# Performance work log

Hardware: AMD Instinct MI355X
Metric: run time of the kernel (lower is better)

## Reference

```python
import jax, jax.numpy as jnp
import numpy as np

H, F, E_SHARED, E_ROUTED, K = 1024, 4096, 1, 8, 2


def setup_inputs() -> dict:
    key = jax.random.key(0)
    ks = jax.random.split(key, 6)
    x = jax.random.normal(ks[0], (4, 2048, H), dtype=jnp.float32)
    s = 0.02
    shared_up = jax.random.normal(ks[1], (E_SHARED, H, F), dtype=jnp.float32) * s
    shared_down = jax.random.normal(ks[2], (E_SHARED, F, H), dtype=jnp.float32) * s
    routed_up = jax.random.normal(ks[3], (E_ROUTED, H, F), dtype=jnp.float32) * s
    routed_down = jax.random.normal(ks[4], (E_ROUTED, F, H), dtype=jnp.float32) * s
    router_w = jax.random.normal(ks[5], (H, E_ROUTED), dtype=jnp.float32) * s
    return {"x": x, "shared_up": shared_up, "shared_down": shared_down,
            "routed_up": routed_up, "routed_down": routed_down, "router_w": router_w}


def _expert(x, w_up, w_down):
    # ExpertBlock: down(gelu(up(x))), exact (erf) gelu as in torch F.gelu default
    h = jax.nn.gelu(jnp.einsum('bsh,hf->bsf', x, w_up), approximate=False)
    return jnp.einsum('bsf,fh->bsh', h, w_down)


def reference(x, shared_up, shared_down, routed_up, routed_down, router_w):
    # shared experts (always active)
    shared_out = jnp.zeros_like(x)
    for i in range(E_SHARED):
        shared_out = shared_out + _expert(x, shared_up[i], shared_down[i])

    # router: softmax over routed experts, then top-k gating
    probs = jax.nn.softmax(jnp.einsum('bsh,he->bse', x, router_w), axis=-1)
    top_k_prob, top_k_idx = jax.lax.top_k(probs, K)  # [B,S,K]
    # per-expert gate = sum of top-k probs assigned to that expert
    onehot = jax.nn.one_hot(top_k_idx, E_ROUTED, dtype=x.dtype)  # [B,S,K,E]
    gates = jnp.einsum('bsk,bske->bse', top_k_prob, onehot)      # [B,S,E]

    routed_out = jnp.zeros_like(x)
    for e in range(E_ROUTED):  # fixed small loop over experts
        y = _expert(x, routed_up[e], routed_down[e])
        routed_out = routed_out + gates[..., e:e + 1] * y

    return shared_out + routed_out + x
```

## Files before the change

### kernel.cpp

```cpp
#include <hip/hip_runtime.h>
#include <cstdint>
#include <cstddef>

#define HD 1024
#define FF 4096
#define TOK 8192
#define NSEG 9
#define ROWS_ROUTED (TOK*2)
#define ROWS_TOT (ROWS_ROUTED + TOK)

typedef __bf16 bf16;
typedef __bf16 bf16x8 __attribute__((ext_vector_type(8)));
typedef __bf16 bf16x4 __attribute__((ext_vector_type(4)));
typedef float  f32x4  __attribute__((ext_vector_type(4)));

__device__ __forceinline__ void stage16(const void* g, void* l) {
  __builtin_amdgcn_global_load_lds((const __attribute__((address_space(1))) void*)g,
                                   (__attribute__((address_space(3))) void*)l,
                                   16, 0, 0);
}

__device__ __forceinline__ unsigned short bf_bits(float v) {
  bf16 b = (bf16)v;
  return __builtin_bit_cast(unsigned short, b);
}

__global__ void k_init_meta(int* meta) {
  int t = threadIdx.x;
  if (t < 64) meta[t] = 0;
}

__global__ void k_convert_x(const float* __restrict__ x, bf16* __restrict__ xbf) {
  int i = blockIdx.x*256 + threadIdx.x;
  float4 v = reinterpret_cast<const float4*>(x)[i];
  ushort4 u;
  u.x = bf_bits(v.x); u.y = bf_bits(v.y); u.z = bf_bits(v.z); u.w = bf_bits(v.w);
  reinterpret_cast<ushort4*>(xbf)[i] = u;
}

__global__ void k_tcvt(const float* __restrict__ routed, const float* __restrict__ shared_,
                       bf16* __restrict__ dst, int R, int C) {
  int e = blockIdx.z;
  const float* src = (e < 8) ? (routed + (size_t)e*R*C) : shared_;
  bf16* d = dst + (size_t)e*R*C;
  __shared__ float lds[64][65];
  int r0 = blockIdx.y*64, c0 = blockIdx.x*64;
  int t = threadIdx.x;
  int tr = t>>4, tc4 = (t&15)*4;
  #pragma unroll
  for (int i=0;i<4;i++) {
    float4 v = *reinterpret_cast<const float4*>(src + (size_t)(r0+tr+i*16)*C + c0 + tc4);
    lds[tr+i*16][tc4+0]=v.x; lds[tr+i*16][tc4+1]=v.y;
    lds[tr+i*16][tc4+2]=v.z; lds[tr+i*16][tc4+3]=v.w;
  }
  __syncthreads();
  #pragma unroll
  for (int i=0;i<4;i++) {
    int oc = tr + i*16;
    ushort4 u;
    u.x = bf_bits(lds[tc4+0][oc]);
    u.y = bf_bits(lds[tc4+1][oc]);
    u.z = bf_bits(lds[tc4+2][oc]);
    u.w = bf_bits(lds[tc4+3][oc]);
    *reinterpret_cast<ushort4*>(d + (size_t)(c0+oc)*R + r0 + tc4) = u;
  }
}

__global__ void k_router(const float* __restrict__ x, const float* __restrict__ rw,
                         int* __restrict__ rtE, float* __restrict__ rtG,
                         int* __restrict__ meta) {
  __shared__ float rwl[HD*8];
  int t = threadIdx.x;
  for (int i=t;i<HD*8/4;i+=256)
    reinterpret_cast<float4*>(rwl)[i] = reinterpret_cast<const float4*>(rw)[i];
  __syncthreads();
  int wv = t>>6, lane = t&63;
  int tk = blockIdx.x*4 + wv;
  const float* xr = x + (size_t)tk*HD;
  float a[8] = {0,0,0,0,0,0,0,0};
  for (int i=0;i<HD/64;i++) {
    int h = lane + i*64;
    float xv = xr[h];
    const float* r = rwl + h*8;
    #pragma unroll
    for (int e=0;e<8;e++) a[e] = fmaf(xv, r[e], a[e]);
  }
  #pragma unroll
  for (int e=0;e<8;e++) {
    for (int s=32;s>0;s>>=1) a[e] += __shfl_xor(a[e], s, 64);
  }
  if (lane==0) {
    float mx = a[0];
    #pragma unroll
    for (int e=1;e<8;e++) mx = fmaxf(mx, a[e]);
    float p[8]; float den = 0.f;
    #pragma unroll
    for (int e=0;e<8;e++) { p[e] = expf(a[e]-mx); den += p[e]; }
    int i0 = 0;
    #pragma unroll
    for (int e=1;e<8;e++) if (p[e] > p[i0]) i0 = e;
    int i1 = (i0==0)?1:0;
    #pragma unroll
    for (int e=0;e<8;e++) if (e!=i0 && p[e] > p[i1]) i1 = e;
    float inv = 1.f/den;
    rtE[tk*2] = i0; rtE[tk*2+1] = i1;
    rtG[tk*2] = p[i0]*inv; rtG[tk*2+1] = p[i1]*inv;
    atomicAdd(&meta[i0], 1);
    atomicAdd(&meta[i1], 1);
  }
}

__global__ void k_prefix(int* meta) {
  if (threadIdx.x == 0) {
    int off = 0;
    for (int e=0;e<8;e++) { meta[16+e] = off; meta[32+e] = meta[e]; off += meta[e]; }
    meta[16+8] = ROWS_ROUTED;
    meta[32+8] = TOK;
  }
}

__global__ void k_scatter(const int* __restrict__ rtE, const float* __restrict__ rtG,
                          int* __restrict__ meta, int* __restrict__ tok,
                          float* __restrict__ gate, int* __restrict__ trow) {
  int t = blockIdx.x*256 + threadIdx.x;
  int e0 = rtE[t*2], e1 = rtE[t*2+1];
  float g0 = rtG[t*2], g1 = rtG[t*2+1];
  int p0 = atomicAdd(&meta[8+e0], 1);
  int r0 = meta[16+e0] + p0;
  tok[r0] = t; gate[r0] = g0; trow[t*2] = r0;
  int p1 = atomicAdd(&meta[8+e1], 1);
  int r1 = meta[16+e1] + p1;
  tok[r1] = t; gate[r1] = g1; trow[t*2+1] = r1;
  tok[ROWS_ROUTED + t] = t; gate[ROWS_ROUTED + t] = 1.0f;
}

__global__ void k_combine(const float* __restrict__ x, const bf16* __restrict__ dbuf,
                          const int* __restrict__ trow, float* __restrict__ out) {
  int tkn = blockIdx.x;
  int t = threadIdx.x;
  int r0 = trow[tkn*2], r1 = trow[tkn*2+1];
  int h = t*4;
  float4 xv = *reinterpret_cast<const float4*>(x + (size_t)tkn*HD + h);
  bf16x4 a = *reinterpret_cast<const bf16x4*>(dbuf + (size_t)(ROWS_ROUTED+tkn)*HD + h);
  bf16x4 b = *reinterpret_cast<const bf16x4*>(dbuf + (size_t)r0*HD + h);
  bf16x4 c = *reinterpret_cast<const bf16x4*>(dbuf + (size_t)r1*HD + h);
  float4 o;
  o.x = xv.x + (float)a[0] + (float)b[0] + (float)c[0];
  o.y = xv.y + (float)a[1] + (float)b[1] + (float)c[1];
  o.z = xv.z + (float)a[2] + (float)b[2] + (float)c[2];
  o.w = xv.w + (float)a[3] + (float)b[3] + (float)c[3];
  *reinterpret_cast<float4*>(out + (size_t)tkn*HD + h) = o;
}


__global__ __launch_bounds__(256,2) void k_gemm_up(
    const bf16* __restrict__ xbf, const bf16* __restrict__ wupT,
    bf16* __restrict__ hbuf, const int* __restrict__ tok,
    const int* __restrict__ meta, int ch, int FC, int ntiles)
{
  int bx = blockIdx.x;
  int bps = 64*ntiles;
  int seg = bx / bps; int rem = bx % bps;
  int mt = rem / ntiles, nt = rem % ntiles;
  int rows = (seg<8)? meta[32+seg] : TOK;
  if (mt*128 >= rows) return;
  int segoff = meta[16+seg];
  int rowbase = mt*128;

  __shared__ __align__(16) bf16 Alds[2][128*32];
  __shared__ __align__(16) bf16 Blds[2][128*32];

  const int t = threadIdx.x;
  const int lane = t & 63, w = t >> 6;

  int lr0 = t>>2, lr1 = 64 + (t>>2);
  int gr0 = rowbase + lr0; if (gr0 >= rows) gr0 = rowbase;
  int gr1 = rowbase + lr1; if (gr1 >= rows) gr1 = rowbase;
  int tok0 = tok[segoff + gr0], tok1 = tok[segoff + gr1];
  int kswz = ((t&3) ^ ((t>>3)&3)) * 8;
  const bf16* gA0 = xbf + (size_t)tok0*HD + kswz;
  const bf16* gA1 = xbf + (size_t)tok1*HD + kswz;
  const bf16* wb = wupT + (size_t)seg*FF*HD;
  int f0 = ch*FC + nt*128;
  const bf16* gB0 = wb + (size_t)(f0 + lr0)*HD + kswz;
  const bf16* gB1 = wb + (size_t)(f0 + lr1)*HD + kswz;

  char* AldsB = (char*)Alds; char* BldsB = (char*)Blds;
  const int stoff = w*1024;

  const int slotb = ((lane>>4) ^ (((lane&15)>>1)&3)) * 16;
  const int Afo = ((w>>1)*64 + (lane&15))*64 + slotb;
  const int Bfo = ((w&1)*64 + (lane&15))*64 + slotb;

  f32x4 acc[4][4] = {};

  stage16(gA0, AldsB + stoff);
  stage16(gA1, AldsB + 4096 + stoff);
  stage16(gB0, BldsB + stoff);
  stage16(gB1, BldsB + 4096 + stoff);
  __syncthreads();

  int cur = 0;
  for (int k0=32; k0<HD; k0+=32) {
    char* an = AldsB + (cur^1)*8192;
    char* bn = BldsB + (cur^1)*8192;
    stage16(gA0 + k0, an + stoff);
    stage16(gA1 + k0, an + 4096 + stoff);
    stage16(gB0 + k0, bn + stoff);
    stage16(gB1 + k0, bn + 4096 + stoff);
    const char* Ab = AldsB + cur*8192 + Afo;
    const char* Bb = BldsB + cur*8192 + Bfo;
    bf16x8 af[4], bfr[4];
    #pragma unroll
    for (int m=0;m<4;m++) af[m]  = *reinterpret_cast<const bf16x8*>(Ab + m*1024);
    #pragma unroll
    for (int n=0;n<4;n++) bfr[n] = *reinterpret_cast<const bf16x8*>(Bb + n*1024);
    #pragma unroll
    for (int m=0;m<4;m++)
      #pragma unroll
      for (int n=0;n<4;n++)
        acc[m][n] = __builtin_amdgcn_mfma_f32_16x16x32_bf16(bfr[n], af[m], acc[m][n], 0,0,0);
    __syncthreads();
    cur ^= 1;
  }
  {
    const char* Ab = AldsB + cur*8192 + Afo;
    const char* Bb = BldsB + cur*8192 + Bfo;
    bf16x8 af[4], bfr[4];
    #pragma unroll
    for (int m=0;m<4;m++) af[m]  = *reinterpret_cast<const bf16x8*>(Ab + m*1024);
    #pragma unroll
    for (int n=0;n<4;n++) bfr[n] = *reinterpret_cast<const bf16x8*>(Bb + n*1024);
    #pragma unroll
    for (int m=0;m<4;m++)
      #pragma unroll
      for (int n=0;n<4;n++)
        acc[m][n] = __builtin_amdgcn_mfma_f32_16x16x32_bf16(bfr[n], af[m], acc[m][n], 0,0,0);
  }

  const int lrm = lane&15, lq = lane>>4;
  #pragma unroll
  for (int m=0;m<4;m++) {
    int rl = (w>>1)*64 + m*16 + lrm;
    int gr = rowbase + rl;
    if (gr >= rows) continue;
    bf16* hrow = hbuf + (size_t)(segoff+gr)*FC + nt*128 + (w&1)*64 + lq*4;
    #pragma unroll
    for (int n=0;n<4;n++) {
      bf16x4 u;
      #pragma unroll
      for (int j=0;j<4;j++) {
        float v = acc[m][n][j];
        v = 0.5f*v*(1.0f + erff(v*0.70710678118654752f));
        u[j] = (bf16)v;
      }
      *reinterpret_cast<bf16x4*>(hrow + n*16) = u;
    }
  }
}

__global__ __launch_bounds__(256,2) void k_gemm_down(
    const bf16* __restrict__ hbuf, const bf16* __restrict__ wdnT,
    bf16* __restrict__ dbuf, const float* __restrict__ gate,
    const int* __restrict__ meta, int ch, int FC, int first)
{
  int bx = blockIdx.x;
  int seg = bx >> 9;
  int rem = bx & 511;
  int mt = rem >> 3, nt = rem & 7;
  int rows = (seg<8)? meta[32+seg] : TOK;
  if (mt*128 >= rows) return;
  int segoff = meta[16+seg];
  int rowbase = mt*128;

  __shared__ __align__(16) bf16 Alds[2][128*32];
  __shared__ __align__(16) bf16 Blds[2][128*32];
  __shared__ float gateL[128];

  const int t = threadIdx.x;
  const int lane = t & 63, w = t >> 6;

  if (t < 128) {
    int gr = rowbase + t; if (gr >= rows) gr = rows - 1;
    gateL[t] = gate[segoff + gr];
  }

  int lr0 = t>>2, lr1 = 64 + (t>>2);
  int kswz = ((t&3) ^ ((t>>3)&3)) * 8;
  const bf16* gA0 = hbuf + (size_t)(segoff + rowbase + lr0)*FC + kswz;
  const bf16* gA1 = hbuf + (size_t)(segoff + rowbase + lr1)*FC + kswz;
  const bf16* wb = wdnT + (size_t)seg*HD*FF;
  int h0 = nt*128;
  const bf16* gB0 = wb + (size_t)(h0 + lr0)*FF + ch*FC + kswz;
  const bf16* gB1 = wb + (size_t)(h0 + lr1)*FF + ch*FC + kswz;

  char* AldsB = (char*)Alds; char* BldsB = (char*)Blds;
  const int stoff = w*1024;

  const int slotb = ((lane>>4) ^ (((lane&15)>>1)&3)) * 16;
  const int Afo = ((w>>1)*64 + (lane&15))*64 + slotb;
  const int Bfo = ((w&1)*64 + (lane&15))*64 + slotb;

  f32x4 acc[4][4] = {};

  stage16(gA0, AldsB + stoff);
  stage16(gA1, AldsB + 4096 + stoff);
  stage16(gB0, BldsB + stoff);
  stage16(gB1, BldsB + 4096 + stoff);
  __syncthreads();

  int cur = 0;
  for (int k0=32; k0<FC; k0+=32) {
    char* an = AldsB + (cur^1)*8192;
    char* bn = BldsB + (cur^1)*8192;
    stage16(gA0 + k0, an + stoff);
    stage16(gA1 + k0, an + 4096 + stoff);
    stage16(gB0 + k0, bn + stoff);
    stage16(gB1 + k0, bn + 4096 + stoff);
    const char* Ab = AldsB + cur*8192 + Afo;
    const char* Bb = BldsB + cur*8192 + Bfo;
    bf16x8 af[4], bfr[4];
    #pragma unroll
    for (int m=0;m<4;m++) af[m]  = *reinterpret_cast<const bf16x8*>(Ab + m*1024);
    #pragma unroll
    for (int n=0;n<4;n++) bfr[n] = *reinterpret_cast<const bf16x8*>(Bb + n*1024);
    #pragma unroll
    for (int m=0;m<4;m++)
      #pragma unroll
      for (int n=0;n<4;n++)
        acc[m][n] = __builtin_amdgcn_mfma_f32_16x16x32_bf16(bfr[n], af[m], acc[m][n], 0,0,0);
    __syncthreads();
    cur ^= 1;
  }
  {
    const char* Ab = AldsB + cur*8192 + Afo;
    const char* Bb = BldsB + cur*8192 + Bfo;
    bf16x8 af[4], bfr[4];
    #pragma unroll
    for (int m=0;m<4;m++) af[m]  = *reinterpret_cast<const bf16x8*>(Ab + m*1024);
    #pragma unroll
    for (int n=0;n<4;n++) bfr[n] = *reinterpret_cast<const bf16x8*>(Bb + n*1024);
    #pragma unroll
    for (int m=0;m<4;m++)
      #pragma unroll
      for (int n=0;n<4;n++)
        acc[m][n] = __builtin_amdgcn_mfma_f32_16x16x32_bf16(bfr[n], af[m], acc[m][n], 0,0,0);
  }

  const int lrm = lane&15, lq = lane>>4;
  #pragma unroll
  for (int m=0;m<4;m++) {
    int rl = (w>>1)*64 + m*16 + lrm;
    int gr = rowbase + rl;
    if (gr >= rows) continue;
    float g = gateL[rl];
    bf16* drow = dbuf + (size_t)(segoff+gr)*HD + nt*128 + (w&1)*64 + lq*4;
    #pragma unroll
    for (int n=0;n<4;n++) {
      bf16x4 u;
      if (first) {
        #pragma unroll
        for (int j=0;j<4;j++) u[j] = (bf16)(acc[m][n][j]*g);
      } else {
        bf16x4 o = *reinterpret_cast<const bf16x4*>(drow + n*16);
        #pragma unroll
        for (int j=0;j<4;j++) u[j] = (bf16)((float)o[j] + acc[m][n][j]*g);
      }
      *reinterpret_cast<bf16x4*>(drow + n*16) = u;
    }
  }
}

struct Layout {
  size_t xbf, wupT, wdnT, hbuf, dbuf, tok, gate, trow, rtE, rtG, meta, total;
};

static inline Layout make_layout(size_t FC) {
  Layout L; size_t o = 0;
  auto al = [&](size_t b){ o = (o+255)&~(size_t)255; size_t r=o; o+=b; return r; };
  L.xbf  = al((size_t)TOK*HD*2);
  L.wupT = al((size_t)NSEG*FF*HD*2);
  L.wdnT = al((size_t)NSEG*FF*HD*2);
  L.hbuf = al((size_t)ROWS_TOT*FC*2);
  L.dbuf = al((size_t)ROWS_TOT*HD*2);
  L.tok  = al((size_t)ROWS_TOT*4);
  L.gate = al((size_t)ROWS_TOT*4);
  L.trow = al((size_t)TOK*2*4);
  L.rtE  = al((size_t)TOK*2*4);
  L.rtG  = al((size_t)TOK*2*4);
  L.meta = al(256*4);
  L.total = o;
  return L;
}

extern "C" void kernel_launch(void* const* d_in, const int* in_sizes, int n_in,
                              void* d_out, int out_size, void* d_ws, size_t ws_size,
                              hipStream_t stream) {
  const float* x           = (const float*)d_in[0];
  const float* shared_up   = (const float*)d_in[1];
  const float* shared_down = (const float*)d_in[2];
  const float* routed_up   = (const float*)d_in[3];
  const float* routed_down = (const float*)d_in[4];
  const float* router_w    = (const float*)d_in[5];
  float* out = (float*)d_out;

  size_t FC = 4096;
  while (FC > 256 && make_layout(FC).total > ws_size) FC >>= 1;
  Layout L = make_layout(FC);

  char* ws = (char*)d_ws;
  bf16*  xbf  = (bf16*)(ws + L.xbf);
  bf16*  wupT = (bf16*)(ws + L.wupT);
  bf16*  wdnT = (bf16*)(ws + L.wdnT);
  bf16*  hbuf = (bf16*)(ws + L.hbuf);
  bf16*  dbuf = (bf16*)(ws + L.dbuf);
  int*   tok  = (int*)(ws + L.tok);
  float* gate = (float*)(ws + L.gate);
  int*   trow = (int*)(ws + L.trow);
  int*   rtE  = (int*)(ws + L.rtE);
  float* rtG  = (float*)(ws + L.rtG);
  int*   meta = (int*)(ws + L.meta);

  k_init_meta<<<1, 64, 0, stream>>>(meta);
  k_convert_x<<<TOK*HD/1024, 256, 0, stream>>>(x, xbf);
  k_tcvt<<<dim3(FF/64, HD/64, NSEG), 256, 0, stream>>>(routed_up, shared_up, wupT, HD, FF);
  k_tcvt<<<dim3(HD/64, FF/64, NSEG), 256, 0, stream>>>(routed_down, shared_down, wdnT, FF, HD);
  k_router<<<TOK/4, 256, 0, stream>>>(x, router_w, rtE, rtG, meta);
  k_prefix<<<1, 64, 0, stream>>>(meta);
  k_scatter<<<TOK/256, 256, 0, stream>>>(rtE, rtG, meta, tok, gate, trow);

  int ntiles = (int)(FC/128);
  int fc = (int)FC;
  for (int ch = 0; ch*fc < FF; ++ch) {
    k_gemm_up<<<NSEG*64*ntiles, 256, 0, stream>>>(xbf, wupT, hbuf, tok, meta, ch, fc, ntiles);
    k_gemm_down<<<NSEG*64*8, 256, 0, stream>>>(hbuf, wdnT, dbuf, gate, meta, ch, fc, ch==0 ? 1 : 0);
  }
  k_combine<<<TOK, 256, 0, stream>>>(x, dbuf, trow, out);
}
```

Baseline: 1.044 ms.

## Enlarge GEMM tiles to 256 rows with 512 threads and triple-buffered LDS pipeline

Both expert GEMMs move to 512-thread blocks with 256-row tiles (256x256 for up, 256x128 for down), and the double-buffered LDS loop becomes a 3-stage pipeline with explicit vmcnt waits, raw barriers and raised wave priority around the MFMA block. The FC chunking loop is removed, so the full 4096-wide hidden buffer is always allocated and the down GEMM writes its output once instead of read-modify-writing per chunk. Larger tiles raise arithmetic intensity and deeper prefetch hides load latency, at the cost of more registers and LDS per block, fewer blocks, and a larger workspace requirement with no fallback if ws_size is too small.

```diff
diff --git a/kernel.cpp b/kernel.cpp
--- a/kernel.cpp
+++ b/kernel.cpp
@@ -8,6 +8,9 @@
 #define NSEG 9
 #define ROWS_ROUTED (TOK*2)
 #define ROWS_TOT (ROWS_ROUTED + TOK)
+
+#define BUF_UP 32768
+#define BUF_DN 24576
 
 typedef __bf16 bf16;
 typedef __bf16 bf16x8 __attribute__((ext_vector_type(8)));
@@ -153,98 +156,87 @@
 }
 
 
-__global__ __launch_bounds__(256,2) void k_gemm_up(
+__global__ __launch_bounds__(512,2) void k_gemm_up(
     const bf16* __restrict__ xbf, const bf16* __restrict__ wupT,
     bf16* __restrict__ hbuf, const int* __restrict__ tok,
-    const int* __restrict__ meta, int ch, int FC, int ntiles)
+    const int* __restrict__ meta)
 {
   int bx = blockIdx.x;
-  int bps = 64*ntiles;
-  int seg = bx / bps; int rem = bx % bps;
-  int mt = rem / ntiles, nt = rem % ntiles;
+  int seg = bx >> 9;
+  int rem = bx & 511;
+  int mt = rem >> 4, nt = rem & 15;
   int rows = (seg<8)? meta[32+seg] : TOK;
-  if (mt*128 >= rows) return;
+  if (mt*256 >= rows) return;
   int segoff = meta[16+seg];
-  int rowbase = mt*128;
-
-  __shared__ __align__(16) bf16 Alds[2][128*32];
-  __shared__ __align__(16) bf16 Blds[2][128*32];
+  int rowbase = mt*256;
+
+  __shared__ __align__(16) char lds[3*BUF_UP];
 
   const int t = threadIdx.x;
   const int lane = t & 63, w = t >> 6;
-
-  int lr0 = t>>2, lr1 = 64 + (t>>2);
-  int gr0 = rowbase + lr0; if (gr0 >= rows) gr0 = rowbase;
-  int gr1 = rowbase + lr1; if (gr1 >= rows) gr1 = rowbase;
-  int tok0 = tok[segoff + gr0], tok1 = tok[segoff + gr1];
+  const int wm = w >> 2, wn = w & 3;
+
+  int ar = t>>2;
   int kswz = ((t&3) ^ ((t>>3)&3)) * 8;
-  const bf16* gA0 = xbf + (size_t)tok0*HD + kswz;
-  const bf16* gA1 = xbf + (size_t)tok1*HD + kswz;
+  int gr0 = rowbase + ar;        if (gr0 >= rows) gr0 = rows-1;
+  int gr1 = rowbase + 128 + ar;  if (gr1 >= rows) gr1 = rows-1;
+  const bf16* gA0 = xbf + (size_t)tok[segoff+gr0]*HD + kswz;
+  const bf16* gA1 = xbf + (size_t)tok[segoff+gr1]*HD + kswz;
   const bf16* wb = wupT + (size_t)seg*FF*HD;
-  int f0 = ch*FC + nt*128;
-  const bf16* gB0 = wb + (size_t)(f0 + lr0)*HD + kswz;
-  const bf16* gB1 = wb + (size_t)(f0 + lr1)*HD + kswz;
-
-  char* AldsB = (char*)Alds; char* BldsB = (char*)Blds;
-  const int stoff = w*1024;
-
-  const int slotb = ((lane>>4) ^ (((lane&15)>>1)&3)) * 16;
-  const int Afo = ((w>>1)*64 + (lane&15))*64 + slotb;
-  const int Bfo = ((w&1)*64 + (lane&15))*64 + slotb;
-
-  f32x4 acc[4][4] = {};
-
-  stage16(gA0, AldsB + stoff);
-  stage16(gA1, AldsB + 4096 + stoff);
-  stage16(gB0, BldsB + stoff);
-  stage16(gB1, BldsB + 4096 + stoff);
-  __syncthreads();
-
-  int cur = 0;
-  for (int k0=32; k0<HD; k0+=32) {
-    char* an = AldsB + (cur^1)*8192;
-    char* bn = BldsB + (cur^1)*8192;
-    stage16(gA0 + k0, an + stoff);
-    stage16(gA1 + k0, an + 4096 + stoff);
-    stage16(gB0 + k0, bn + stoff);
-    stage16(gB1 + k0, bn + 4096 + stoff);
-    const char* Ab = AldsB + cur*8192 + Afo;
-    const char* Bb = BldsB + cur*8192 + Bfo;
-    bf16x8 af[4], bfr[4];
-    #pragma unroll
-    for (int m=0;m<4;m++) af[m]  = *reinterpret_cast<const bf16x8*>(Ab + m*1024);
-    #pragma unroll
-    for (int n=0;n<4;n++) bfr[n] = *reinterpret_cast<const bf16x8*>(Bb + n*1024);
-    #pragma unroll
-    for (int m=0;m<4;m++)
+  int f0 = nt*256;
+  const bf16* gB0 = wb + (size_t)(f0 + ar)*HD + kswz;
+  const bf16* gB1 = wb + (size_t)(f0 + 128 + ar)*HD + kswz;
+  const int dA0 = t*16, dA1 = 8192 + t*16, dB0 = 16384 + t*16, dB1 = 24576 + t*16;
+
+  const int sx = ((lane>>4) ^ (((lane&15)>>1)&3)) * 16;
+  const int Afo = (wm*128 + (lane&15))*64 + sx;
+  const int Bfo = 16384 + (wn*64 + (lane&15))*64 + sx;
+
+  f32x4 acc[8][4] = {};
+
+  stage16(gA0,    lds + dA0); stage16(gA1,    lds + dA1);
+  stage16(gB0,    lds + dB0); stage16(gB1,    lds + dB1);
+  stage16(gA0+32, lds + BUF_UP + dA0); stage16(gA1+32, lds + BUF_UP + dA1);
+  stage16(gB0+32, lds + BUF_UP + dB0); stage16(gB1+32, lds + BUF_UP + dB1);
+  asm volatile("s_waitcnt vmcnt(4)" ::: "memory");
+  __builtin_amdgcn_s_barrier();
+  __builtin_amdgcn_sched_barrier(0);
+
+  int cur = 0, nxt = 2;
+  for (int kt = 0; kt < HD/32; ++kt) {
+    if (kt + 2 < HD/32) {
+      int ko = (kt+2)*32;
+      char* nb = lds + nxt*BUF_UP;
+      stage16(gA0+ko, nb + dA0); stage16(gA1+ko, nb + dA1);
+      stage16(gB0+ko, nb + dB0); stage16(gB1+ko, nb + dB1);
+    }
+    const char* cb = lds + cur*BUF_UP;
+    bf16x8 af[8], bfr[4];
+    #pragma unroll
+    for (int m=0;m<8;m++) af[m]  = *reinterpret_cast<const bf16x8*>(cb + Afo + m*1024);
+    #pragma unroll
+    for (int n=0;n<4;n++) bfr[n] = *reinterpret_cast<const bf16x8*>(cb + Bfo + n*1024);
+    __builtin_amdgcn_s_setprio(1);
+    #pragma unroll
+    for (int m=0;m<8;m++)
       #pragma unroll
       for (int n=0;n<4;n++)
         acc[m][n] = __builtin_amdgcn_mfma_f32_16x16x32_bf16(bfr[n], af[m], acc[m][n], 0,0,0);
-    __syncthreads();
-    cur ^= 1;
-  }
-  {
-    const char* Ab = AldsB + cur*8192 + Afo;
-    const char* Bb = BldsB + cur*8192 + Bfo;
-    bf16x8 af[4], bfr[4];
-    #pragma unroll
-    for (int m=0;m<4;m++) af[m]  = *reinterpret_cast<const bf16x8*>(Ab + m*1024);
-    #pragma unroll
-    for (int n=0;n<4;n++) bfr[n] = *reinterpret_cast<const bf16x8*>(Bb + n*1024);
-    #pragma unroll
-    for (int m=0;m<4;m++)
-      #pragma unroll
-      for (int n=0;n<4;n++)
-        acc[m][n] = __builtin_amdgcn_mfma_f32_16x16x32_bf16(bfr[n], af[m], acc[m][n], 0,0,0);
+    __builtin_amdgcn_s_setprio(0);
+    if (kt + 2 < HD/32)       asm volatile("s_waitcnt vmcnt(4)" ::: "memory");
+    else if (kt + 1 < HD/32)  asm volatile("s_waitcnt vmcnt(0)" ::: "memory");
+    __builtin_amdgcn_s_barrier();
+    __builtin_amdgcn_sched_barrier(0);
+    cur = (cur==2)?0:cur+1; nxt = (nxt==2)?0:nxt+1;
   }
 
   const int lrm = lane&15, lq = lane>>4;
   #pragma unroll
-  for (int m=0;m<4;m++) {
-    int rl = (w>>1)*64 + m*16 + lrm;
+  for (int m=0;m<8;m++) {
+    int rl = wm*128 + m*16 + lrm;
     int gr = rowbase + rl;
     if (gr >= rows) continue;
-    bf16* hrow = hbuf + (size_t)(segoff+gr)*FC + nt*128 + (w&1)*64 + lq*4;
+    bf16* hrow = hbuf + (size_t)(segoff+gr)*FF + nt*256 + wn*64 + lq*4;
     #pragma unroll
     for (int n=0;n<4;n++) {
       bf16x4 u;
@@ -259,113 +251,94 @@
   }
 }
 
-__global__ __launch_bounds__(256,2) void k_gemm_down(
+__global__ __launch_bounds__(512,2) void k_gemm_down(
     const bf16* __restrict__ hbuf, const bf16* __restrict__ wdnT,
     bf16* __restrict__ dbuf, const float* __restrict__ gate,
-    const int* __restrict__ meta, int ch, int FC, int first)
+    const int* __restrict__ meta)
 {
   int bx = blockIdx.x;
-  int seg = bx >> 9;
-  int rem = bx & 511;
+  int seg = bx >> 8;
+  int rem = bx & 255;
   int mt = rem >> 3, nt = rem & 7;
   int rows = (seg<8)? meta[32+seg] : TOK;
-  if (mt*128 >= rows) return;
+  if (mt*256 >= rows) return;
   int segoff = meta[16+seg];
-  int rowbase = mt*128;
-
-  __shared__ __align__(16) bf16 Alds[2][128*32];
-  __shared__ __align__(16) bf16 Blds[2][128*32];
-  __shared__ float gateL[128];
+  int rowbase = mt*256;
+
+  __shared__ __align__(16) char lds[3*BUF_DN];
+  __shared__ float gateL[256];
 
   const int t = threadIdx.x;
   const int lane = t & 63, w = t >> 6;
-
-  if (t < 128) {
+  const int wm = w >> 2, wn = w & 3;
+
+  if (t < 256) {
     int gr = rowbase + t; if (gr >= rows) gr = rows - 1;
     gateL[t] = gate[segoff + gr];
   }
 
-  int lr0 = t>>2, lr1 = 64 + (t>>2);
+  int ar = t>>2;
   int kswz = ((t&3) ^ ((t>>3)&3)) * 8;
-  const bf16* gA0 = hbuf + (size_t)(segoff + rowbase + lr0)*FC + kswz;
-  const bf16* gA1 = hbuf + (size_t)(segoff + rowbase + lr1)*FC + kswz;
+  const bf16* gA0 = hbuf + (size_t)(segoff + rowbase + ar)*FF + kswz;
+  const bf16* gA1 = hbuf + (size_t)(segoff + rowbase + 128 + ar)*FF + kswz;
   const bf16* wb = wdnT + (size_t)seg*HD*FF;
   int h0 = nt*128;
-  const bf16* gB0 = wb + (size_t)(h0 + lr0)*FF + ch*FC + kswz;
-  const bf16* gB1 = wb + (size_t)(h0 + lr1)*FF + ch*FC + kswz;
-
-  char* AldsB = (char*)Alds; char* BldsB = (char*)Blds;
-  const int stoff = w*1024;
-
-  const int slotb = ((lane>>4) ^ (((lane&15)>>1)&3)) * 16;
-  const int Afo = ((w>>1)*64 + (lane&15))*64 + slotb;
-  const int Bfo = ((w&1)*64 + (lane&15))*64 + slotb;
-
-  f32x4 acc[4][4] = {};
-
-  stage16(gA0, AldsB + stoff);
-  stage16(gA1, AldsB + 4096 + stoff);
-  stage16(gB0, BldsB + stoff);
-  stage16(gB1, BldsB + 4096 + stoff);
-  __syncthreads();
-
-  int cur = 0;
-  for (int k0=32; k0<FC; k0+=32) {
-    char* an = AldsB + (cur^1)*8192;
-    char* bn = BldsB + (cur^1)*8192;
-    stage16(gA0 + k0, an + stoff);
-    stage16(gA1 + k0, an + 4096 + stoff);
-    stage16(gB0 + k0, bn + stoff);
-    stage16(gB1 + k0, bn + 4096 + stoff);
-    const char* Ab = AldsB + cur*8192 + Afo;
-    const char* Bb = BldsB + cur*8192 + Bfo;
-    bf16x8 af[4], bfr[4];
-    #pragma unroll
-    for (int m=0;m<4;m++) af[m]  = *reinterpret_cast<const bf16x8*>(Ab + m*1024);
-    #pragma unroll
-    for (int n=0;n<4;n++) bfr[n] = *reinterpret_cast<const bf16x8*>(Bb + n*1024);
-    #pragma unroll
-    for (int m=0;m<4;m++)
+  const bf16* gB0 = wb + (size_t)(h0 + ar)*FF + kswz;
+  const int dA0 = t*16, dA1 = 8192 + t*16, dB0 = 16384 + t*16;
+
+  const int sx = ((lane>>4) ^ (((lane&15)>>1)&3)) * 16;
+  const int Afo = (wm*128 + (lane&15))*64 + sx;
+  const int Bfo = 16384 + (wn*32 + (lane&15))*64 + sx;
+
+  f32x4 acc[8][2] = {};
+
+  stage16(gA0,    lds + dA0); stage16(gA1,    lds + dA1); stage16(gB0,    lds + dB0);
+  stage16(gA0+32, lds + BUF_DN + dA0); stage16(gA1+32, lds + BUF_DN + dA1);
+  stage16(gB0+32, lds + BUF_DN + dB0);
+  asm volatile("s_waitcnt vmcnt(3)" ::: "memory");
+  __builtin_amdgcn_s_barrier();
+  __builtin_amdgcn_sched_barrier(0);
+
+  int cur = 0, nxt = 2;
+  for (int kt = 0; kt < FF/32; ++kt) {
+    if (kt + 2 < FF/32) {
+      int ko = (kt+2)*32;
+      char* nb = lds + nxt*BUF_DN;
+      stage16(gA0+ko, nb + dA0); stage16(gA1+ko, nb + dA1); stage16(gB0+ko, nb + dB0);
+    }
+    const char* cb = lds + cur*BUF_DN;
+    bf16x8 af[8], bfr[2];
+    #pragma unroll
+    for (int m=0;m<8;m++) af[m]  = *reinterpret_cast<const bf16x8*>(cb + Afo + m*1024);
+    #pragma unroll
+    for (int n=0;n<2;n++) bfr[n] = *reinterpret_cast<const bf16x8*>(cb + Bfo + n*1024);
+    __builtin_amdgcn_s_setprio(1);
+    #pragma unroll
+    for (int m=0;m<8;m++)
       #pragma unroll
-      for (int n=0;n<4;n++)
+      for (int n=0;n<2;n++)
         acc[m][n] = __builtin_amdgcn_mfma_f32_16x16x32_bf16(bfr[n], af[m], acc[m][n], 0,0,0);
-    __syncthreads();
-    cur ^= 1;
-  }
-  {
-    const char* Ab = AldsB + cur*8192 + Afo;
-    const char* Bb = BldsB + cur*8192 + Bfo;
-    bf16x8 af[4], bfr[4];
-    #pragma unroll
-    for (int m=0;m<4;m++) af[m]  = *reinterpret_cast<const bf16x8*>(Ab + m*1024);
-    #pragma unroll
-    for (int n=0;n<4;n++) bfr[n] = *reinterpret_cast<const bf16x8*>(Bb + n*1024);
-    #pragma unroll
-    for (int m=0;m<4;m++)
-      #pragma unroll
-      for (int n=0;n<4;n++)
-        acc[m][n] = __builtin_amdgcn_mfma_f32_16x16x32_bf16(bfr[n], af[m], acc[m][n], 0,0,0);
+    __builtin_amdgcn_s_setprio(0);
+    if (kt + 2 < FF/32)       asm volatile("s_waitcnt vmcnt(3)" ::: "memory");
+    else if (kt + 1 < FF/32)  asm volatile("s_waitcnt vmcnt(0)" ::: "memory");
+    __builtin_amdgcn_s_barrier();
+    __builtin_amdgcn_sched_barrier(0);
+    cur = (cur==2)?0:cur+1; nxt = (nxt==2)?0:nxt+1;
   }
 
   const int lrm = lane&15, lq = lane>>4;
   #pragma unroll
-  for (int m=0;m<4;m++) {
-    int rl = (w>>1)*64 + m*16 + lrm;
+  for (int m=0;m<8;m++) {
+    int rl = wm*128 + m*16 + lrm;
     int gr = rowbase + rl;
     if (gr >= rows) continue;
     float g = gateL[rl];
-    bf16* drow = dbuf + (size_t)(segoff+gr)*HD + nt*128 + (w&1)*64 + lq*4;
-    #pragma unroll
-    for (int n=0;n<4;n++) {
+    bf16* drow = dbuf + (size_t)(segoff+gr)*HD + nt*128 + wn*32 + lq*4;
+    #pragma unroll
+    for (int n=0;n<2;n++) {
       bf16x4 u;
-      if (first) {
-        #pragma unroll
-        for (int j=0;j<4;j++) u[j] = (bf16)(acc[m][n][j]*g);
-      } else {
-        bf16x4 o = *reinterpret_cast<const bf16x4*>(drow + n*16);
-        #pragma unroll
-        for (int j=0;j<4;j++) u[j] = (bf16)((float)o[j] + acc[m][n][j]*g);
-      }
+      #pragma unroll
+      for (int j=0;j<4;j++) u[j] = (bf16)(acc[m][n][j]*g);
       *reinterpret_cast<bf16x4*>(drow + n*16) = u;
     }
   }
@@ -375,13 +348,13 @@
   size_t xbf, wupT, wdnT, hbuf, dbuf, tok, gate, trow, rtE, rtG, meta, total;
 };
 
-static inline Layout make_layout(size_t FC) {
+static inline Layout make_layout() {
   Layout L; size_t o = 0;
   auto al = [&](size_t b){ o = (o+255)&~(size_t)255; size_t r=o; o+=b; return r; };
   L.xbf  = al((size_t)TOK*HD*2);
   L.wupT = al((size_t)NSEG*FF*HD*2);
   L.wdnT = al((size_t)NSEG*FF*HD*2);
-  L.hbuf = al((size_t)ROWS_TOT*FC*2);
+  L.hbuf = al((size_t)ROWS_TOT*FF*2);
   L.dbuf = al((size_t)ROWS_TOT*HD*2);
   L.tok  = al((size_t)ROWS_TOT*4);
   L.gate = al((size_t)ROWS_TOT*4);
@@ -404,10 +377,7 @@
   const float* router_w    = (const float*)d_in[5];
   float* out = (float*)d_out;
 
-  size_t FC = 4096;
-  while (FC > 256 && make_layout(FC).total > ws_size) FC >>= 1;
-  Layout L = make_layout(FC);
-
+  Layout L = make_layout();
   char* ws = (char*)d_ws;
   bf16*  xbf  = (bf16*)(ws + L.xbf);
   bf16*  wupT = (bf16*)(ws + L.wupT);
@@ -429,11 +399,7 @@
   k_prefix<<<1, 64, 0, stream>>>(meta);
   k_scatter<<<TOK/256, 256, 0, stream>>>(rtE, rtG, meta, tok, gate, trow);
 
-  int ntiles = (int)(FC/128);
-  int fc = (int)FC;
-  for (int ch = 0; ch*fc < FF; ++ch) {
-    k_gemm_up<<<NSEG*64*ntiles, 256, 0, stream>>>(xbf, wupT, hbuf, tok, meta, ch, fc, ntiles);
-    k_gemm_down<<<NSEG*64*8, 256, 0, stream>>>(hbuf, wdnT, dbuf, gate, meta, ch, fc, ch==0 ? 1 : 0);
-  }
+  k_gemm_up<<<NSEG*512, 512, 0, stream>>>(xbf, wupT, hbuf, tok, meta);
+  k_gemm_down<<<NSEG*256, 512, 0, stream>>>(hbuf, wdnT, dbuf, gate, meta);
   k_combine<<<TOK, 256, 0, stream>>>(x, dbuf, trow, out);
 }
```

Result: slower. 1.207 ms (+15.7%).

## Drop F-chunking and remap block indices across XCDs for GEMM locality

Applied to the files above, without the earlier changes.

Removes the workspace-driven F-chunk loop so each GEMM runs once over the full 4096 intermediate dimension. This eliminates the read-modify-write accumulation of the down-projection output across chunks and the repeated bf16 rounding it caused. It also adds a block-index remap so that neighbouring tiles land on the same XCD, which is meant to improve L2 reuse of weights and activations. In exchange it assumes the workspace always fits the full hidden buffer and drops the fallback for smaller workspaces.

```diff
diff --git a/kernel.cpp b/kernel.cpp
--- a/kernel.cpp
+++ b/kernel.cpp
@@ -23,6 +23,10 @@
 __device__ __forceinline__ unsigned short bf_bits(float v) {
   bf16 b = (bf16)v;
   return __builtin_bit_cast(unsigned short, b);
+}
+
+__device__ __forceinline__ int xcd_remap(int d) {
+  return (((d >> 6) << 3) + (d & 7)) * 8 + ((d >> 3) & 7);
 }
 
 __global__ void k_init_meta(int* meta) {
@@ -156,12 +160,12 @@
 __global__ __launch_bounds__(256,2) void k_gemm_up(
     const bf16* __restrict__ xbf, const bf16* __restrict__ wupT,
     bf16* __restrict__ hbuf, const int* __restrict__ tok,
-    const int* __restrict__ meta, int ch, int FC, int ntiles)
+    const int* __restrict__ meta)
 {
-  int bx = blockIdx.x;
-  int bps = 64*ntiles;
-  int seg = bx / bps; int rem = bx % bps;
-  int mt = rem / ntiles, nt = rem % ntiles;
+  int bx = xcd_remap(blockIdx.x);
+  int seg = bx >> 11;
+  int rem = bx & 2047;
+  int mt = rem >> 5, nt = rem & 31;
   int rows = (seg<8)? meta[32+seg] : TOK;
   if (mt*128 >= rows) return;
   int segoff = meta[16+seg];
@@ -181,7 +185,7 @@
   const bf16* gA0 = xbf + (size_t)tok0*HD + kswz;
   const bf16* gA1 = xbf + (size_t)tok1*HD + kswz;
   const bf16* wb = wupT + (size_t)seg*FF*HD;
-  int f0 = ch*FC + nt*128;
+  int f0 = nt*128;
   const bf16* gB0 = wb + (size_t)(f0 + lr0)*HD + kswz;
   const bf16* gB1 = wb + (size_t)(f0 + lr1)*HD + kswz;
 
@@ -244,7 +248,7 @@
     int rl = (w>>1)*64 + m*16 + lrm;
     int gr = rowbase + rl;
     if (gr >= rows) continue;
-    bf16* hrow = hbuf + (size_t)(segoff+gr)*FC + nt*128 + (w&1)*64 + lq*4;
+    bf16* hrow = hbuf + (size_t)(segoff+gr)*FF + nt*128 + (w&1)*64 + lq*4;
     #pragma unroll
     for (int n=0;n<4;n++) {
       bf16x4 u;
@@ -262,9 +266,9 @@
 __global__ __launch_bounds__(256,2) void k_gemm_down(
     const bf16* __restrict__ hbuf, const bf16* __restrict__ wdnT,
     bf16* __restrict__ dbuf, const float* __restrict__ gate,
-    const int* __restrict__ meta, int ch, int FC, int first)
+    const int* __restrict__ meta)
 {
-  int bx = blockIdx.x;
+  int bx = xcd_remap(blockIdx.x);
   int seg = bx >> 9;
   int rem = bx & 511;
   int mt = rem >> 3, nt = rem & 7;
@@ -287,12 +291,12 @@
 
   int lr0 = t>>2, lr1 = 64 + (t>>2);
   int kswz = ((t&3) ^ ((t>>3)&3)) * 8;
-  const bf16* gA0 = hbuf + (size_t)(segoff + rowbase + lr0)*FC + kswz;
-  const bf16* gA1 = hbuf + (size_t)(segoff + rowbase + lr1)*FC + kswz;
+  const bf16* gA0 = hbuf + (size_t)(segoff + rowbase + lr0)*FF + kswz;
+  const bf16* gA1 = hbuf + (size_t)(segoff + rowbase + lr1)*FF + kswz;
   const bf16* wb = wdnT + (size_t)seg*HD*FF;
   int h0 = nt*128;
-  const bf16* gB0 = wb + (size_t)(h0 + lr0)*FF + ch*FC + kswz;
-  const bf16* gB1 = wb + (size_t)(h0 + lr1)*FF + ch*FC + kswz;
+  const bf16* gB0 = wb + (size_t)(h0 + lr0)*FF + kswz;
+  const bf16* gB1 = wb + (size_t)(h0 + lr1)*FF + kswz;
 
   char* AldsB = (char*)Alds; char* BldsB = (char*)Blds;
   const int stoff = w*1024;
@@ -310,7 +314,7 @@
   __syncthreads();
 
   int cur = 0;
-  for (int k0=32; k0<FC; k0+=32) {
+  for (int k0=32; k0<FF; k0+=32) {
     char* an = AldsB + (cur^1)*8192;
     char* bn = BldsB + (cur^1)*8192;
     stage16(gA0 + k0, an + stoff);
@@ -358,14 +362,8 @@
     #pragma unroll
     for (int n=0;n<4;n++) {
       bf16x4 u;
-      if (first) {
-        #pragma unroll
-        for (int j=0;j<4;j++) u[j] = (bf16)(acc[m][n][j]*g);
-      } else {
-        bf16x4 o = *reinterpret_cast<const bf16x4*>(drow + n*16);
-        #pragma unroll
-        for (int j=0;j<4;j++) u[j] = (bf16)((float)o[j] + acc[m][n][j]*g);
-      }
+      #pragma unroll
+      for (int j=0;j<4;j++) u[j] = (bf16)(acc[m][n][j]*g);
       *reinterpret_cast<bf16x4*>(drow + n*16) = u;
     }
   }
@@ -375,13 +373,13 @@
   size_t xbf, wupT, wdnT, hbuf, dbuf, tok, gate, trow, rtE, rtG, meta, total;
 };
 
-static inline Layout make_layout(size_t FC) {
+static inline Layout make_layout() {
   Layout L; size_t o = 0;
   auto al = [&](size_t b){ o = (o+255)&~(size_t)255; size_t r=o; o+=b; return r; };
   L.xbf  = al((size_t)TOK*HD*2);
   L.wupT = al((size_t)NSEG*FF*HD*2);
   L.wdnT = al((size_t)NSEG*FF*HD*2);
-  L.hbuf = al((size_t)ROWS_TOT*FC*2);
+  L.hbuf = al((size_t)ROWS_TOT*FF*2);
   L.dbuf = al((size_t)ROWS_TOT*HD*2);
   L.tok  = al((size_t)ROWS_TOT*4);
   L.gate = al((size_t)ROWS_TOT*4);
@@ -404,10 +402,7 @@
   const float* router_w    = (const float*)d_in[5];
   float* out = (float*)d_out;
 
-  size_t FC = 4096;
-  while (FC > 256 && make_layout(FC).total > ws_size) FC >>= 1;
-  Layout L = make_layout(FC);
-
+  Layout L = make_layout();
   char* ws = (char*)d_ws;
   bf16*  xbf  = (bf16*)(ws + L.xbf);
   bf16*  wupT = (bf16*)(ws + L.wupT);
@@ -429,11 +424,7 @@
   k_prefix<<<1, 64, 0, stream>>>(meta);
   k_scatter<<<TOK/256, 256, 0, stream>>>(rtE, rtG, meta, tok, gate, trow);
 
-  int ntiles = (int)(FC/128);
-  int fc = (int)FC;
-  for (int ch = 0; ch*fc < FF; ++ch) {
-    k_gemm_up<<<NSEG*64*ntiles, 256, 0, stream>>>(xbf, wupT, hbuf, tok, meta, ch, fc, ntiles);
-    k_gemm_down<<<NSEG*64*8, 256, 0, stream>>>(hbuf, wdnT, dbuf, gate, meta, ch, fc, ch==0 ? 1 : 0);
-  }
+  k_gemm_up<<<NSEG*64*32, 256, 0, stream>>>(xbf, wupT, hbuf, tok, meta);
+  k_gemm_down<<<NSEG*64*8, 256, 0, stream>>>(hbuf, wdnT, dbuf, gate, meta);
   k_combine<<<TOK, 256, 0, stream>>>(x, dbuf, trow, out);
 }
```

Result: faster. 1.004 ms (-3.7%).
